# Kernel tuning notes

Measured on AMD Instinct MI355X. Metric: run time of the kernel, lower is better.

## Reference

```python
import jax, jax.numpy as jnp
import numpy as np

B, C, D, E = 2048, 64, 1024, 128
P_INT = 0.0  # p_int=0 -> intervention mask is all zeros (deterministic)


def setup_inputs() -> dict:
    key = jax.random.key(0)
    ks = jax.random.split(key, 16)
    s = lambda k, shape, fan: jax.random.normal(k, shape, jnp.float32) * (1.0 / np.sqrt(fan))
    return {
        "x": jax.random.normal(ks[0], (B, D), jnp.float32),
        "c_int": jax.random.uniform(ks[1], (B, C), jnp.float32),
        # stacked per-concept scorer MLP: Linear(D,D) -> ReLU -> Linear(D,1) -> Sigmoid
        "W1": s(ks[2], (C, D, D), D), "b1": jnp.zeros((C, D), jnp.float32),
        "w2": s(ks[3], (C, D), D), "b2": jnp.zeros((C,), jnp.float32),
        # stacked per-concept embed layer: Linear(D+1, D+1) -> ReLU
        "Wl": s(ks[4], (C, D + 1, D + 1), D + 1), "bl": jnp.zeros((C, D + 1), jnp.float32),
        # shared heads
        "Wmu": s(ks[5], (D + 1, E), D + 1), "bmu": jnp.zeros((E,), jnp.float32),
        "Wlv": s(ks[6], (D + 1, E), D + 1), "blv": jnp.zeros((E,), jnp.float32),
        "proto_pos": jax.random.normal(ks[7], (C, E), jnp.float32),
        "proto_neg": jax.random.normal(ks[8], (C, E), jnp.float32),
    }


def reference(x, c_int, W1, b1, w2, b2, Wl, bl, Wmu, bmu, Wlv, blv, proto_pos, proto_neg):
    # Concept scorers (all concepts batched as one grouped GEMM).
    h = jax.nn.relu(jnp.einsum("bd,cdk->bck", x, W1) + b1)          # [B,C,D]
    c_pred = jax.nn.sigmoid(jnp.einsum("bck,ck->bc", h, w2) + b2)    # [B,C]
    # Per-concept embedding layer on [x ; c_pred].
    xc = jnp.concatenate(
        [jnp.broadcast_to(x[:, None, :], (x.shape[0], C, D)), c_pred[..., None]], axis=-1
    )                                                                # [B,C,D+1]
    emb = jax.nn.relu(jnp.einsum("bck,ckj->bcj", xc, Wl) + bl)       # [B,C,D+1]
    mu = jnp.einsum("bcj,je->bce", emb, Wmu) + bmu                   # [B,C,E]
    logvar = jnp.einsum("bcj,je->bce", emb, Wlv) + blv               # [B,C,E]
    c_emb = mu  # eval mode: no reparameterization noise
    # Intervention blend (mask ~ Bernoulli(p_int); p_int=0 -> zeros, deterministic)
    mask = jnp.zeros_like(c_pred)                                    # [B,C]
    cp = mask * c_int + (1.0 - mask) * c_pred                        # [B,C]
    proto = cp[..., None] * proto_pos + (1.0 - cp[..., None]) * proto_neg  # [B,C,E]
    c_emb = mask[..., None] * proto + (1.0 - mask[..., None]) * c_emb
    return (c_pred, c_emb, mu, logvar)
```

## Files before the change

kernel.cpp:

```cpp
#include <hip/hip_runtime.h>
#include <hip/hip_bf16.h>
#include <cstdint>
#include <cstddef>

#define OFF_CE 131072ull
#define OFF_MU (131072ull + 16777216ull)
#define OFF_LV (131072ull + 33554432ull)

using bf16x8 = __attribute__((ext_vector_type(8))) __bf16;
using s16x8  = __attribute__((ext_vector_type(8))) short;
using f32x4  = __attribute__((ext_vector_type(4))) float;

__device__ __forceinline__ unsigned short f2bf(float x) {
  unsigned u = __builtin_bit_cast(unsigned, x);
  return (unsigned short)((u + 0x7FFFu + ((u >> 16) & 1u)) >> 16);
}
__device__ __forceinline__ float bf2f(unsigned short h) {
  unsigned u = ((unsigned)h) << 16;
  return __builtin_bit_cast(float, u);
}
__device__ __forceinline__ void async16(const void* g, void* l) {
  __builtin_amdgcn_global_load_lds(
      (const __attribute__((address_space(1))) void*)g,
      (__attribute__((address_space(3))) void*)l, 16, 0, 0);
}
__device__ __forceinline__ f32x4 nt_load4(const float* p4) {
  return __builtin_nontemporal_load((const f32x4*)p4);
}

struct PX {
  const float *Wl, *Wmu, *Wlv, *b2, *presum, *w2l, *bl1024, *Wlcolf;
  const unsigned short *xb;
  unsigned short *WlT, *WheadT;
  float *whead1024f, *e1024, *pred;
};

template <int ALIGNED, int NT>
__device__ __forceinline__ void tile_tr64(const float* __restrict__ src, int stride,
                                          unsigned short* __restrict__ dst, int t256,
                                          float (*t)[68]) {
#pragma unroll
  for (int i = 0; i < 4; ++i) {
    const int row = (t256 >> 4) + (i << 4);
    const int col4 = (t256 & 15) << 2;
    const float* sp = src + (size_t)row * stride + col4;
    f32x4 v;
    if constexpr (ALIGNED && NT) {
      v = nt_load4(sp);
    } else if constexpr (ALIGNED) {
      v = *(const f32x4*)sp;
    } else if constexpr (NT) {
      v.x = __builtin_nontemporal_load(sp);
      v.y = __builtin_nontemporal_load(sp + 1);
      v.z = __builtin_nontemporal_load(sp + 2);
      v.w = __builtin_nontemporal_load(sp + 3);
    } else {
      v.x = sp[0]; v.y = sp[1]; v.z = sp[2]; v.w = sp[3];
    }
    *(f32x4*)&t[row][col4] = v;
  }
  __syncthreads();
  const int n = t256 & 63;
#pragma unroll
  for (int pq = 0; pq < 2; ++pq) {
    const int k8 = ((t256 >> 6) << 3) + (pq << 5);
    unsigned short tmp[8];
#pragma unroll
    for (int j = 0; j < 8; ++j) tmp[j] = f2bf(t[k8 + j][n]);
    *(uint4*)(dst + (size_t)n * 1024 + k8) = *(uint4*)tmp;
  }
}

__global__ __launch_bounds__(256) void prep1_k(const float* __restrict__ W1,
                                               const float* __restrict__ x,
                                               const float* __restrict__ Wl,
                                               const float* __restrict__ bl,
                                               unsigned short* __restrict__ xb,
                                               unsigned short* __restrict__ W1T,
                                               float* __restrict__ wlastf,
                                               float* __restrict__ blpf,
                                               float* __restrict__ Wlcolf,
                                               float* __restrict__ w2l,
                                               float* __restrict__ bl1024) {
  __shared__ float t[64][68];
  const int bid = blockIdx.x;
  const int tid = threadIdx.x;
  if (bid < 16384) {
    const int c = bid >> 8, kt = (bid >> 4) & 15, nt = bid & 15;
    tile_tr64<1, 1>(W1 + ((size_t)c << 20) + ((size_t)(kt << 6) << 10) + (nt << 6), 1024,
                    W1T + ((size_t)c << 20) + ((size_t)(nt << 6) << 10) + (kt << 6), tid, t);
  } else if (bid < 17408) {
    const int idx = (bid - 16384) * 256 + tid;
    f32x4 a = nt_load4(x + (size_t)idx * 8);
    f32x4 b = nt_load4(x + (size_t)idx * 8 + 4);
    unsigned w0 = f2bf(a.x) | ((unsigned)f2bf(a.y) << 16);
    unsigned w1 = f2bf(a.z) | ((unsigned)f2bf(a.w) << 16);
    unsigned w2 = f2bf(b.x) | ((unsigned)f2bf(b.y) << 16);
    unsigned w3 = f2bf(b.z) | ((unsigned)f2bf(b.w) << 16);
    ((uint4*)xb)[idx] = make_uint4(w0, w1, w2, w3);
  } else {
    const int idx = (bid - 17408) * 256 + tid;
    const int c = idx >> 10, j = idx & 1023;
    const float* src = Wl + (size_t)c * 1050625;
    wlastf[idx] = __builtin_nontemporal_load(&src[(size_t)1024 * 1025 + j]);
    blpf[idx]   = bl[(size_t)c * 1025 + j];
    Wlcolf[idx] = __builtin_nontemporal_load(&src[(size_t)j * 1025 + 1024]);
    if (j == 0) {
      w2l[c]    = src[(size_t)1024 * 1025 + 1024];
      bl1024[c] = bl[(size_t)c * 1025 + 1024];
    }
  }
}

__device__ void tail_work(int e, int tid, char* lds, const PX& p) {
  if (e < 4096) {
    const int g = tid >> 8, t256 = tid & 255;
    const int tau0 = (e << 2) + (g << 1);
    float (*tA)[68] = (float(*)[68])(lds + g * 34816);
    float (*tB)[68] = (float(*)[68])(lds + g * 34816 + 17408);
    const int c0 = tau0 >> 8, kt0 = (tau0 >> 4) & 15, nt0 = tau0 & 15;
    const int tau1 = tau0 + 1;
    const int c1 = tau1 >> 8, kt1 = (tau1 >> 4) & 15, nt1 = tau1 & 15;
    const float* srcA = p.Wl + (size_t)c0 * 1050625 + (size_t)(kt0 << 6) * 1025 + (nt0 << 6);
    const float* srcB = p.Wl + (size_t)c1 * 1050625 + (size_t)(kt1 << 6) * 1025 + (nt1 << 6);
    unsigned short* dstA = p.WlT + ((size_t)c0 << 20) + ((size_t)(nt0 << 6) << 10) + (kt0 << 6);
    unsigned short* dstB = p.WlT + ((size_t)c1 << 20) + ((size_t)(nt1 << 6) << 10) + (kt1 << 6);
    const int row = t256 >> 4;
    const int col4 = (t256 & 15) << 2;
    f32x4 vA[4], vB[4];
#pragma unroll
    for (int i = 0; i < 4; ++i) {
      const float* q = srcA + (size_t)(row + (i << 4)) * 1025 + col4;
      vA[i].x = __builtin_nontemporal_load(q);
      vA[i].y = __builtin_nontemporal_load(q + 1);
      vA[i].z = __builtin_nontemporal_load(q + 2);
      vA[i].w = __builtin_nontemporal_load(q + 3);
    }
#pragma unroll
    for (int i = 0; i < 4; ++i) {
      const float* q = srcB + (size_t)(row + (i << 4)) * 1025 + col4;
      vB[i].x = __builtin_nontemporal_load(q);
      vB[i].y = __builtin_nontemporal_load(q + 1);
      vB[i].z = __builtin_nontemporal_load(q + 2);
      vB[i].w = __builtin_nontemporal_load(q + 3);
    }
#pragma unroll
    for (int i = 0; i < 4; ++i) *(f32x4*)&tA[row + (i << 4)][col4] = vA[i];
    __syncthreads();
#pragma unroll
    for (int i = 0; i < 4; ++i) *(f32x4*)&tB[row + (i << 4)][col4] = vB[i];
    const int n = t256 & 63;
#pragma unroll
    for (int pq = 0; pq < 2; ++pq) {
      const int k8 = ((t256 >> 6) << 3) + (pq << 5);
      unsigned short tmp[8];
#pragma unroll
      for (int j = 0; j < 8; ++j) tmp[j] = f2bf(tA[k8 + j][n]);
      *(uint4*)(dstA + (size_t)n * 1024 + k8) = *(uint4*)tmp;
    }
    __syncthreads();
#pragma unroll
    for (int pq = 0; pq < 2; ++pq) {
      const int k8 = ((t256 >> 6) << 3) + (pq << 5);
      unsigned short tmp[8];
#pragma unroll
      for (int j = 0; j < 8; ++j) tmp[j] = f2bf(tB[k8 + j][n]);
      *(uint4*)(dstB + (size_t)n * 1024 + k8) = *(uint4*)tmp;
    }
    return;
  }
  if (e < 4608) {
    const int we = e - 4096;
    const int idx = we * 512 + tid;
    const int rr = idx >> 10, k = idx & 1023;
    float v = (rr < 128) ? p.Wmu[(size_t)k * 128 + rr] : p.Wlv[(size_t)k * 128 + (rr - 128)];
    p.WheadT[idx] = f2bf(v);
    if (we == 0 && tid < 256)
      p.whead1024f[tid] = (tid < 128) ? p.Wmu[131072 + tid] : p.Wlv[131072 + (tid - 128)];
    return;
  }
  const int b = e - 4608;
  const int w = tid >> 6, lane = tid & 63;
  const unsigned short* xr = p.xb + ((size_t)b << 10) + lane * 16;
  s16x8 xv0 = *(const s16x8*)xr;
  s16x8 xv1 = *(const s16x8*)(xr + 8);
  float xf[16];
#pragma unroll
  for (int i = 0; i < 8; ++i) {
    xf[i] = bf2f((unsigned short)xv0[i]);
    xf[8 + i] = bf2f((unsigned short)xv1[i]);
  }
#pragma unroll
  for (int q = 0; q < 8; ++q) {
    const int c = (q << 3) + w;
    const float* wr = p.Wlcolf + (c << 10) + lane * 16;
    float s = 0.f;
#pragma unroll
    for (int q4 = 0; q4 < 4; ++q4) {
      f32x4 wv = *(const f32x4*)(wr + q4 * 4);
      s += xf[q4 * 4 + 0] * wv.x + xf[q4 * 4 + 1] * wv.y +
           xf[q4 * 4 + 2] * wv.z + xf[q4 * 4 + 3] * wv.w;
    }
#pragma unroll
    for (int off = 32; off; off >>= 1) s += __shfl_xor(s, off);
    if (lane == 0) ((float*)p.presum)[(c << 11) + b] = s;
  }
}


#define BAR() __builtin_amdgcn_s_barrier()
#define LGKM0() do { asm volatile("s_waitcnt lgkmcnt(0)" ::: "memory"); \
                     __builtin_amdgcn_sched_barrier(0); } while (0)
#define VM4() asm volatile("s_waitcnt vmcnt(4)" ::: "memory")
#define VM0() asm volatile("s_waitcnt vmcnt(0)" ::: "memory")

#define STAGEA(h, tt, bidx) do { _Pragma("unroll") for (int q_ = 0; q_ < 2; ++q_) \
  async16(Asrc[q_] + ((size_t)(h) * 128) * K + (size_t)(tt) * 64, \
          &sA[bidx][(h) * 8192 + chnk[q_]]); } while (0)
#define STAGEB(h, tt, bidx) do { _Pragma("unroll") for (int q_ = 0; q_ < 2; ++q_) \
  async16(Bsrc[q_] + ((size_t)(h) * 128) * K + (size_t)(tt) * 64, \
          &sB[bidx][(h) * 8192 + chnk[q_]]); } while (0)

#define LOADA(mh, bidx) do { _Pragma("unroll") for (int i_ = 0; i_ < 4; ++i_) { \
  const int ro_ = ((mh) * 128 + wm64 + i_ * 16 + l15) << 6; \
  a[i_][0] = *(const bf16x8*)&sA[bidx][ro_ + ccx0]; \
  a[i_][1] = *(const bf16x8*)&sA[bidx][ro_ + ccx1]; } } while (0)

#define LOADB(nh, bb, bidx) do { _Pragma("unroll") for (int j_ = 0; j_ < 2; ++j_) { \
  const int ro_ = ((nh) * 128 + wn32 + j_ * 16 + l15) << 6; \
  bb[j_][0] = *(const bf16x8*)&sB[bidx][ro_ + ccx0]; \
  bb[j_][1] = *(const bf16x8*)&sB[bidx][ro_ + ccx1]; } } while (0)

#define MMAQ(mh, nh, bb) do { _Pragma("unroll") for (int i_ = 0; i_ < 4; ++i_) \
  _Pragma("unroll") for (int j_ = 0; j_ < 2; ++j_) { \
    acc[(mh)*4+i_][(nh)*2+j_] = __builtin_amdgcn_mfma_f32_16x16x32_bf16( \
        a[i_][0], bb[j_][0], acc[(mh)*4+i_][(nh)*2+j_], 0, 0, 0); \
    acc[(mh)*4+i_][(nh)*2+j_] = __builtin_amdgcn_mfma_f32_16x16x32_bf16( \
        a[i_][1], bb[j_][1], acc[(mh)*4+i_][(nh)*2+j_], 0, 0, 0); \
  } } while (0)

#define KSTEP(t_, cb_, nb_) do { \
    LOADA(0, cb_); LOADB(0, b0, cb_); STAGEA(0, (t_) + 1, nb_); \
    BAR(); LGKM0(); \
    __builtin_amdgcn_s_setprio(1); MMAQ(0, 0, b0); __builtin_amdgcn_s_setprio(0); \
    VM4(); BAR(); \
    LOADB(1, b1, cb_); STAGEB(0, (t_) + 1, nb_); \
    BAR(); LGKM0(); \
    __builtin_amdgcn_s_setprio(1); MMAQ(0, 1, b1); __builtin_amdgcn_s_setprio(0); \
    VM4(); BAR(); \
    LOADA(1, cb_); STAGEB(1, (t_) + 1, nb_); \
    BAR(); LGKM0(); \
    __builtin_amdgcn_s_setprio(1); MMAQ(1, 1, b1); __builtin_amdgcn_s_setprio(0); \
    BAR(); \
    STAGEA(1, (t_) + 1, nb_); \
    BAR(); \
    __builtin_amdgcn_s_setprio(1); MMAQ(1, 0, b0); __builtin_amdgcn_s_setprio(0); \
    VM4(); BAR(); \
  } while (0)

template <int MODE, int K>
__global__ __launch_bounds__(512, 2) void gemm8p_k(
    const unsigned short* __restrict__ A, const unsigned short* __restrict__ BT,
    const float* __restrict__ e0, const float* __restrict__ e1,
    const float* __restrict__ e2, const float* __restrict__ e3,
    unsigned short* __restrict__ obf, float* __restrict__ ofl, PX p) {
  __shared__ unsigned short sA[2][16384];
  __shared__ unsigned short sB[2][16384];

  constexpr int GX = (MODE == 2) ? 1 : 4;
  constexpr int GY = (MODE == 2) ? 512 : 8;
  constexpr int NWG = GX * GY * ((MODE == 2) ? 1 : 64);

  const int tid = threadIdx.x;

  int rbid;
  if constexpr (MODE == 0) {
    const int bidR = blockIdx.x;
    if (bidR >= 2048) { tail_work(bidR - 2048, tid, (char*)&sA[0][0], p); return; }
    rbid = bidR;
  } else {
    rbid = blockIdx.x + GX * (blockIdx.y + GY * blockIdx.z);
  }

  const int lane = tid & 63;
  const int wid = tid >> 6;
  const int wm = wid >> 2, wn = wid & 3;
  const int l15 = lane & 15, l4 = lane >> 4;
  const int wm64 = wm << 6, wn32 = wn << 5;

  const int bid = (rbid & 7) * (NWG >> 3) + (rbid >> 3);
  const int bx = bid % GX;
  const int by = (bid / GX) % GY;
  const int c = bid / (GX * GY);

  const int n0 = bx << 8;
  const int m0 = by << 8;

  const unsigned short* Ab = A;
  const unsigned short* Bb;
  if constexpr (MODE == 2) Bb = BT;
  else                     Bb = BT + ((size_t)c << 20);

  int rloc[2], csrc[2], chnk[2];
  const unsigned short* Asrc[2];
  const unsigned short* Bsrc[2];
#pragma unroll
  for (int q = 0; q < 2; ++q) {
    const int s = ((wid << 1) + q) * 64 + lane;
    rloc[q] = s >> 3;
    csrc[q] = ((s & 7) ^ ((s >> 3) & 7)) << 3;
    chnk[q] = ((wid << 1) + q) << 9;
    Asrc[q] = Ab + (size_t)(m0 + rloc[q]) * K + csrc[q];
    Bsrc[q] = Bb + (size_t)(n0 + rloc[q]) * K + csrc[q];
  }

  const int xorv = l15 & 7;
  const int ccx0 = (l4 ^ xorv) << 3;
  const int ccx1 = ((4 + l4) ^ xorv) << 3;

  f32x4 acc[8][4];
#pragma unroll
  for (int i = 0; i < 8; ++i)
#pragma unroll
    for (int j = 0; j < 4; ++j) acc[i][j] = (f32x4)(0.f);

  bf16x8 a[4][2], b0[2][2], b1[2][2];

  static_assert(K == 1024, "schedule assumes 16 K-tiles");

  STAGEA(0, 0, 0); STAGEB(0, 0, 0); STAGEB(1, 0, 0); STAGEA(1, 0, 0);
  VM0();
  BAR();

#pragma unroll 1
  for (int tt = 0; tt < 7; ++tt) {
    const int t0 = tt << 1;
    KSTEP(t0, 0, 1);
    KSTEP(t0 + 1, 1, 0);
  }
  KSTEP(14, 0, 1);

  {
    VM0();
    BAR();
    LOADA(0, 1);
    LOADB(0, b0, 1);
    LGKM0();
    __builtin_amdgcn_s_setprio(1);
    MMAQ(0, 0, b0);
    __builtin_amdgcn_s_setprio(0);
    LOADB(1, b1, 1);
    LGKM0();
    __builtin_amdgcn_s_setprio(1);
    MMAQ(0, 1, b1);
    __builtin_amdgcn_s_setprio(0);
    LOADA(1, 1);
    LGKM0();
    __builtin_amdgcn_s_setprio(1);
    MMAQ(1, 1, b1);
    MMAQ(1, 0, b0);
    __builtin_amdgcn_s_setprio(0);
  }

  int coln[2][2];
#pragma unroll
  for (int nh = 0; nh < 2; ++nh)
#pragma unroll
    for (int j = 0; j < 2; ++j) coln[nh][j] = n0 + nh * 128 + wn32 + j * 16 + l15;

  if constexpr (MODE == 0) {
    float bias[2][2], w2v[2][2];
#pragma unroll
    for (int nh = 0; nh < 2; ++nh)
#pragma unroll
      for (int j = 0; j < 2; ++j) {
        bias[nh][j] = e0[(c << 10) + coln[nh][j]];
        w2v[nh][j]  = e1[(c << 10) + coln[nh][j]];
      }
    float* partL = (float*)&sA[0][0];
#pragma unroll
    for (int mh = 0; mh < 2; ++mh)
#pragma unroll
      for (int i = 0; i < 4; ++i)
#pragma unroll
        for (int rr = 0; rr < 4; ++rr) {
          float s = 0.f;
#pragma unroll
          for (int nh = 0; nh < 2; ++nh)
#pragma unroll
            for (int j = 0; j < 2; ++j) {
              float v = fmaxf(acc[mh * 4 + i][nh * 2 + j][rr] + bias[nh][j], 0.f);
              s += v * w2v[nh][j];
            }
          s += __shfl_xor(s, 1); s += __shfl_xor(s, 2);
          s += __shfl_xor(s, 4); s += __shfl_xor(s, 8);
          if (l15 == 0) partL[wid * 128 + mh * 64 + i * 16 + (l4 << 2) + rr] = s;
        }
    __syncthreads();
    if (tid < 256) {
      const int r = tid;
      const int mh_ = r >> 7, wmr = (r >> 6) & 1, low = r & 63;
      float s2 = 0.f;
#pragma unroll
      for (int wn2 = 0; wn2 < 4; ++wn2) s2 += partL[(wmr * 4 + wn2) * 128 + mh_ * 64 + low];
      ofl[(((size_t)(bx << 6) + c) << 11) + m0 + r] = s2;
    }
  } else if constexpr (MODE == 1) {
    float* cpL = (float*)&sA[0][0];
    if (tid < 256) {
      const int b = m0 + tid;
      float s = p.b2[c];
#pragma unroll
      for (int q = 0; q < 4; ++q) s += e2[(((size_t)(q << 6) + c) << 11) + b];
      float pv = 1.f / (1.f + expf(-s));
      cpL[tid] = pv;
      if (bx == 0) {
        p.pred[((size_t)b << 6) + c] = pv;
        p.e1024[(c << 11) + b] =
            fmaxf(p.presum[(c << 11) + b] + pv * p.w2l[c] + p.bl1024[c], 0.f);
      }
    }
    __syncthreads();
    float wl4[2][2], bb4[2][2];
#pragma unroll
    for (int nh = 0; nh < 2; ++nh)
#pragma unroll
      for (int j = 0; j < 2; ++j) {
        wl4[nh][j] = e0[(c << 10) + coln[nh][j]];
        bb4[nh][j] = e1[(c << 10) + coln[nh][j]];
      }
#pragma unroll
    for (int mh = 0; mh < 2; ++mh)
#pragma unroll
      for (int i = 0; i < 4; ++i)
#pragma unroll
        for (int rr = 0; rr < 4; ++rr) {
          const int rl = mh * 128 + wm64 + i * 16 + (l4 << 2) + rr;
          const int row = m0 + rl;
          const float cp = cpL[rl];
          unsigned short* orow = obf + (((size_t)(c << 11) + row) << 10);
#pragma unroll
          for (int nh = 0; nh < 2; ++nh)
#pragma unroll
            for (int j = 0; j < 2; ++j) {
              float v = acc[mh * 4 + i][nh * 2 + j][rr] + cp * wl4[nh][j] + bb4[nh][j];
              orow[coln[nh][j]] = f2bf(fmaxf(v, 0.f));
            }
        }
  } else {
    float bias[2][2], wh[2][2];
#pragma unroll
    for (int nh = 0; nh < 2; ++nh)
#pragma unroll
      for (int j = 0; j < 2; ++j) {
        bias[nh][j] = (nh == 0) ? e0[coln[0][j]] : e1[coln[1][j] - 128];
        wh[nh][j]   = e3[coln[nh][j]];
      }
#pragma unroll
    for (int mh = 0; mh < 2; ++mh)
#pragma unroll
      for (int i = 0; i < 4; ++i)
#pragma unroll
        for (int rr = 0; rr < 4; ++rr) {
          const int rid = m0 + mh * 128 + wm64 + i * 16 + (l4 << 2) + rr;
          const int cc = rid >> 11, b = rid & 2047;
          const float ev = e2[rid];
          const size_t ib = (((size_t)b << 6) + cc) << 7;
#pragma unroll
          for (int j = 0; j < 2; ++j) {
            float v = acc[mh * 4 + i][j][rr] + bias[0][j] + ev * wh[0][j];
            ofl[OFF_MU + ib + coln[0][j]] = v;
            ofl[OFF_CE + ib + coln[0][j]] = v;
          }
#pragma unroll
          for (int j = 0; j < 2; ++j) {
            float v = acc[mh * 4 + i][2 + j][rr] + bias[1][j] + ev * wh[1][j];
            ofl[OFF_LV + ib + (coln[1][j] - 128)] = v;
          }
        }
  }
}


extern "C" void kernel_launch(void* const* d_in, const int* in_sizes, int n_in,
                              void* d_out, int out_size, void* d_ws, size_t ws_size,
                              hipStream_t stream) {
  const float* x   = (const float*)d_in[0];
  const float* W1  = (const float*)d_in[2];
  const float* b1  = (const float*)d_in[3];
  const float* w2  = (const float*)d_in[4];
  const float* b2  = (const float*)d_in[5];
  const float* Wl  = (const float*)d_in[6];
  const float* bl  = (const float*)d_in[7];
  const float* Wmu = (const float*)d_in[8];
  const float* bmu = (const float*)d_in[9];
  const float* Wlv = (const float*)d_in[10];
  const float* blv = (const float*)d_in[11];
  float* out = (float*)d_out;

  char* ws = (char*)d_ws;
  size_t off = 0;
  auto take = [&](size_t bytes) { char* r = ws + off; off += bytes; return r; };
  unsigned short* xb     = (unsigned short*)take(4194304);
  unsigned short* W1T    = (unsigned short*)take(134217728);
  unsigned short* WlT    = (unsigned short*)take(134217728);
  float* wlastf          = (float*)take(262144);
  float* blpf            = (float*)take(262144);
  float* Wlcolf          = (float*)take(262144);
  float* w2l             = (float*)take(512);
  float* bl1024          = (float*)take(512);
  unsigned short* WheadT = (unsigned short*)take(524288);
  float* whead1024f      = (float*)take(1024);
  float* presum          = (float*)take(524288);
  float* spart           = (float*)take(2097152);
  float* e1024f          = (float*)take(524288);
  unsigned short* emb    = (unsigned short*)take(268435456);

  PX p;
  p.Wl = Wl; p.Wmu = Wmu; p.Wlv = Wlv; p.b2 = b2;
  p.presum = presum; p.w2l = w2l; p.bl1024 = bl1024; p.Wlcolf = Wlcolf;
  p.xb = xb; p.WlT = WlT; p.WheadT = WheadT;
  p.whead1024f = whead1024f; p.e1024 = e1024f; p.pred = out;

  prep1_k<<<17664, 256, 0, stream>>>(W1, x, Wl, bl, xb, W1T, wlastf, blpf, Wlcolf, w2l, bl1024);
  gemm8p_k<0, 1024><<<8704, 512, 0, stream>>>(xb, W1T, b1, w2, nullptr, nullptr,
                                              nullptr, spart, p);
  gemm8p_k<1, 1024><<<dim3(4, 8, 64), 512, 0, stream>>>(xb, WlT, wlastf, blpf, spart, nullptr,
                                                        emb, nullptr, p);
  gemm8p_k<2, 1024><<<dim3(1, 512, 1), 512, 0, stream>>>(emb, WheadT, bmu, blv, e1024f,
                                                         whead1024f, nullptr, out, p);
}
```

Before: 932.3 us.

## Split Wl transpose tail work out of GEMM into separate kernel; pair W1 tiles

Moves the Wl transpose, head-weight conversion and presum work out of the tail blocks of the first GEMM launch into a standalone kernel that runs between the two grouped GEMMs. Each block of the W1 prep kernel now has 512 threads and transposes two pairs of tiles, which cuts the block count. The goal is to keep low-occupancy transpose blocks from sharing the GEMM's 2-blocks-per-CU launch bounds and LDS footprint. The cost is an extra kernel launch and giving up any overlap of the memory-bound transpose with the compute-bound GEMM.

```diff
diff --git a/kernel.cpp b/kernel.cpp
--- a/kernel.cpp
+++ b/kernel.cpp
@@ -29,49 +29,68 @@
 }
 
 struct PX {
-  const float *Wl, *Wmu, *Wlv, *b2, *presum, *w2l, *bl1024, *Wlcolf;
-  const unsigned short *xb;
-  unsigned short *WlT, *WheadT;
-  float *whead1024f, *e1024, *pred;
+  const float *b2, *presum, *w2l, *bl1024;
+  float *e1024, *pred;
 };
 
-template <int ALIGNED, int NT>
-__device__ __forceinline__ void tile_tr64(const float* __restrict__ src, int stride,
-                                          unsigned short* __restrict__ dst, int t256,
-                                          float (*t)[68]) {
+template <int ALIGNED>
+__device__ __forceinline__ void tile_tr64_pair(
+    const float* __restrict__ srcA, const float* __restrict__ srcB, int stride,
+    unsigned short* __restrict__ dstA, unsigned short* __restrict__ dstB,
+    int t256, float (*tA)[68], float (*tB)[68]) {
+  const int row = t256 >> 4;
+  const int col4 = (t256 & 15) << 2;
+  f32x4 vA[4], vB[4];
 #pragma unroll
   for (int i = 0; i < 4; ++i) {
-    const int row = (t256 >> 4) + (i << 4);
-    const int col4 = (t256 & 15) << 2;
-    const float* sp = src + (size_t)row * stride + col4;
-    f32x4 v;
-    if constexpr (ALIGNED && NT) {
-      v = nt_load4(sp);
-    } else if constexpr (ALIGNED) {
-      v = *(const f32x4*)sp;
-    } else if constexpr (NT) {
-      v.x = __builtin_nontemporal_load(sp);
-      v.y = __builtin_nontemporal_load(sp + 1);
-      v.z = __builtin_nontemporal_load(sp + 2);
-      v.w = __builtin_nontemporal_load(sp + 3);
+    const float* q = srcA + (size_t)(row + (i << 4)) * stride + col4;
+    if constexpr (ALIGNED) {
+      vA[i] = nt_load4(q);
     } else {
-      v.x = sp[0]; v.y = sp[1]; v.z = sp[2]; v.w = sp[3];
-    }
-    *(f32x4*)&t[row][col4] = v;
-  }
+      vA[i].x = __builtin_nontemporal_load(q);
+      vA[i].y = __builtin_nontemporal_load(q + 1);
+      vA[i].z = __builtin_nontemporal_load(q + 2);
+      vA[i].w = __builtin_nontemporal_load(q + 3);
+    }
+  }
+#pragma unroll
+  for (int i = 0; i < 4; ++i) {
+    const float* q = srcB + (size_t)(row + (i << 4)) * stride + col4;
+    if constexpr (ALIGNED) {
+      vB[i] = nt_load4(q);
+    } else {
+      vB[i].x = __builtin_nontemporal_load(q);
+      vB[i].y = __builtin_nontemporal_load(q + 1);
+      vB[i].z = __builtin_nontemporal_load(q + 2);
+      vB[i].w = __builtin_nontemporal_load(q + 3);
+    }
+  }
+#pragma unroll
+  for (int i = 0; i < 4; ++i) *(f32x4*)&tA[row + (i << 4)][col4] = vA[i];
   __syncthreads();
+#pragma unroll
+  for (int i = 0; i < 4; ++i) *(f32x4*)&tB[row + (i << 4)][col4] = vB[i];
   const int n = t256 & 63;
 #pragma unroll
   for (int pq = 0; pq < 2; ++pq) {
     const int k8 = ((t256 >> 6) << 3) + (pq << 5);
     unsigned short tmp[8];
 #pragma unroll
-    for (int j = 0; j < 8; ++j) tmp[j] = f2bf(t[k8 + j][n]);
-    *(uint4*)(dst + (size_t)n * 1024 + k8) = *(uint4*)tmp;
-  }
-}
-
-__global__ __launch_bounds__(256) void prep1_k(const float* __restrict__ W1,
+    for (int j = 0; j < 8; ++j) tmp[j] = f2bf(tA[k8 + j][n]);
+    *(uint4*)(dstA + (size_t)n * 1024 + k8) = *(uint4*)tmp;
+  }
+  __syncthreads();
+#pragma unroll
+  for (int pq = 0; pq < 2; ++pq) {
+    const int k8 = ((t256 >> 6) << 3) + (pq << 5);
+    unsigned short tmp[8];
+#pragma unroll
+    for (int j = 0; j < 8; ++j) tmp[j] = f2bf(tB[k8 + j][n]);
+    *(uint4*)(dstB + (size_t)n * 1024 + k8) = *(uint4*)tmp;
+  }
+}
+
+__global__ __launch_bounds__(512) void prep1_k(const float* __restrict__ W1,
                                                const float* __restrict__ x,
                                                const float* __restrict__ Wl,
                                                const float* __restrict__ bl,
@@ -82,15 +101,23 @@
                                                float* __restrict__ Wlcolf,
                                                float* __restrict__ w2l,
                                                float* __restrict__ bl1024) {
-  __shared__ float t[64][68];
+  __shared__ float t[4][64][68];
   const int bid = blockIdx.x;
   const int tid = threadIdx.x;
-  if (bid < 16384) {
-    const int c = bid >> 8, kt = (bid >> 4) & 15, nt = bid & 15;
-    tile_tr64<1, 1>(W1 + ((size_t)c << 20) + ((size_t)(kt << 6) << 10) + (nt << 6), 1024,
-                    W1T + ((size_t)c << 20) + ((size_t)(nt << 6) << 10) + (kt << 6), tid, t);
-  } else if (bid < 17408) {
-    const int idx = (bid - 16384) * 256 + tid;
+  if (bid < 4096) {
+    const int g = tid >> 8, t256 = tid & 255;
+    const int tau0 = (bid << 2) + (g << 1);
+    const int c0 = tau0 >> 8, kt0 = (tau0 >> 4) & 15, nt0 = tau0 & 15;
+    const int tau1 = tau0 + 1;
+    const int c1 = tau1 >> 8, kt1 = (tau1 >> 4) & 15, nt1 = tau1 & 15;
+    tile_tr64_pair<1>(
+        W1 + ((size_t)c0 << 20) + ((size_t)(kt0 << 6) << 10) + (nt0 << 6),
+        W1 + ((size_t)c1 << 20) + ((size_t)(kt1 << 6) << 10) + (nt1 << 6), 1024,
+        W1T + ((size_t)c0 << 20) + ((size_t)(nt0 << 6) << 10) + (kt0 << 6),
+        W1T + ((size_t)c1 << 20) + ((size_t)(nt1 << 6) << 10) + (kt1 << 6),
+        t256, t[g << 1], t[(g << 1) + 1]);
+  } else if (bid < 4608) {
+    const int idx = (bid - 4096) * 512 + tid;
     f32x4 a = nt_load4(x + (size_t)idx * 8);
     f32x4 b = nt_load4(x + (size_t)idx * 8 + 4);
     unsigned w0 = f2bf(a.x) | ((unsigned)f2bf(a.y) << 16);
@@ -99,7 +126,7 @@
     unsigned w3 = f2bf(b.z) | ((unsigned)f2bf(b.w) << 16);
     ((uint4*)xb)[idx] = make_uint4(w0, w1, w2, w3);
   } else {
-    const int idx = (bid - 17408) * 256 + tid;
+    const int idx = (bid - 4608) * 512 + tid;
     const int c = idx >> 10, j = idx & 1023;
     const float* src = Wl + (size_t)c * 1050625;
     wlastf[idx] = __builtin_nontemporal_load(&src[(size_t)1024 * 1025 + j]);
@@ -112,98 +139,65 @@
   }
 }
 
-__device__ void tail_work(int e, int tid, char* lds, const PX& p) {
-  if (e < 4096) {
+__global__ __launch_bounds__(512) void wl2_k(const float* __restrict__ Wl,
+                                             const float* __restrict__ Wmu,
+                                             const float* __restrict__ Wlv,
+                                             const unsigned short* __restrict__ xb,
+                                             const float* __restrict__ Wlcolf,
+                                             unsigned short* __restrict__ WlT,
+                                             unsigned short* __restrict__ WheadT,
+                                             float* __restrict__ whead1024f,
+                                             float* __restrict__ presum) {
+  __shared__ float t[4][64][68];
+  const int bid = blockIdx.x;
+  const int tid = threadIdx.x;
+  if (bid < 4096) {
     const int g = tid >> 8, t256 = tid & 255;
-    const int tau0 = (e << 2) + (g << 1);
-    float (*tA)[68] = (float(*)[68])(lds + g * 34816);
-    float (*tB)[68] = (float(*)[68])(lds + g * 34816 + 17408);
+    const int tau0 = (bid << 2) + (g << 1);
     const int c0 = tau0 >> 8, kt0 = (tau0 >> 4) & 15, nt0 = tau0 & 15;
     const int tau1 = tau0 + 1;
     const int c1 = tau1 >> 8, kt1 = (tau1 >> 4) & 15, nt1 = tau1 & 15;
-    const float* srcA = p.Wl + (size_t)c0 * 1050625 + (size_t)(kt0 << 6) * 1025 + (nt0 << 6);
-    const float* srcB = p.Wl + (size_t)c1 * 1050625 + (size_t)(kt1 << 6) * 1025 + (nt1 << 6);
-    unsigned short* dstA = p.WlT + ((size_t)c0 << 20) + ((size_t)(nt0 << 6) << 10) + (kt0 << 6);
-    unsigned short* dstB = p.WlT + ((size_t)c1 << 20) + ((size_t)(nt1 << 6) << 10) + (kt1 << 6);
-    const int row = t256 >> 4;
-    const int col4 = (t256 & 15) << 2;
-    f32x4 vA[4], vB[4];
-#pragma unroll
-    for (int i = 0; i < 4; ++i) {
-      const float* q = srcA + (size_t)(row + (i << 4)) * 1025 + col4;
-      vA[i].x = __builtin_nontemporal_load(q);
-      vA[i].y = __builtin_nontemporal_load(q + 1);
-      vA[i].z = __builtin_nontemporal_load(q + 2);
-      vA[i].w = __builtin_nontemporal_load(q + 3);
-    }
-#pragma unroll
-    for (int i = 0; i < 4; ++i) {
-      const float* q = srcB + (size_t)(row + (i << 4)) * 1025 + col4;
-      vB[i].x = __builtin_nontemporal_load(q);
-      vB[i].y = __builtin_nontemporal_load(q + 1);
-      vB[i].z = __builtin_nontemporal_load(q + 2);
-      vB[i].w = __builtin_nontemporal_load(q + 3);
-    }
-#pragma unroll
-    for (int i = 0; i < 4; ++i) *(f32x4*)&tA[row + (i << 4)][col4] = vA[i];
-    __syncthreads();
-#pragma unroll
-    for (int i = 0; i < 4; ++i) *(f32x4*)&tB[row + (i << 4)][col4] = vB[i];
-    const int n = t256 & 63;
-#pragma unroll
-    for (int pq = 0; pq < 2; ++pq) {
-      const int k8 = ((t256 >> 6) << 3) + (pq << 5);
-      unsigned short tmp[8];
-#pragma unroll
-      for (int j = 0; j < 8; ++j) tmp[j] = f2bf(tA[k8 + j][n]);
-      *(uint4*)(dstA + (size_t)n * 1024 + k8) = *(uint4*)tmp;
-    }
-    __syncthreads();
-#pragma unroll
-    for (int pq = 0; pq < 2; ++pq) {
-      const int k8 = ((t256 >> 6) << 3) + (pq << 5);
-      unsigned short tmp[8];
-#pragma unroll
-      for (int j = 0; j < 8; ++j) tmp[j] = f2bf(tB[k8 + j][n]);
-      *(uint4*)(dstB + (size_t)n * 1024 + k8) = *(uint4*)tmp;
-    }
-    return;
-  }
-  if (e < 4608) {
-    const int we = e - 4096;
+    tile_tr64_pair<0>(
+        Wl + (size_t)c0 * 1050625 + (size_t)(kt0 << 6) * 1025 + (nt0 << 6),
+        Wl + (size_t)c1 * 1050625 + (size_t)(kt1 << 6) * 1025 + (nt1 << 6), 1025,
+        WlT + ((size_t)c0 << 20) + ((size_t)(nt0 << 6) << 10) + (kt0 << 6),
+        WlT + ((size_t)c1 << 20) + ((size_t)(nt1 << 6) << 10) + (kt1 << 6),
+        t256, t[g << 1], t[(g << 1) + 1]);
+  } else if (bid < 4608) {
+    const int we = bid - 4096;
     const int idx = we * 512 + tid;
     const int rr = idx >> 10, k = idx & 1023;
-    float v = (rr < 128) ? p.Wmu[(size_t)k * 128 + rr] : p.Wlv[(size_t)k * 128 + (rr - 128)];
-    p.WheadT[idx] = f2bf(v);
+    float v = (rr < 128) ? Wmu[(size_t)k * 128 + rr] : Wlv[(size_t)k * 128 + (rr - 128)];
+    WheadT[idx] = f2bf(v);
     if (we == 0 && tid < 256)
-      p.whead1024f[tid] = (tid < 128) ? p.Wmu[131072 + tid] : p.Wlv[131072 + (tid - 128)];
-    return;
-  }
-  const int b = e - 4608;
-  const int w = tid >> 6, lane = tid & 63;
-  const unsigned short* xr = p.xb + ((size_t)b << 10) + lane * 16;
-  s16x8 xv0 = *(const s16x8*)xr;
-  s16x8 xv1 = *(const s16x8*)(xr + 8);
-  float xf[16];
-#pragma unroll
-  for (int i = 0; i < 8; ++i) {
-    xf[i] = bf2f((unsigned short)xv0[i]);
-    xf[8 + i] = bf2f((unsigned short)xv1[i]);
-  }
-#pragma unroll
-  for (int q = 0; q < 8; ++q) {
-    const int c = (q << 3) + w;
-    const float* wr = p.Wlcolf + (c << 10) + lane * 16;
-    float s = 0.f;
-#pragma unroll
-    for (int q4 = 0; q4 < 4; ++q4) {
-      f32x4 wv = *(const f32x4*)(wr + q4 * 4);
-      s += xf[q4 * 4 + 0] * wv.x + xf[q4 * 4 + 1] * wv.y +
-           xf[q4 * 4 + 2] * wv.z + xf[q4 * 4 + 3] * wv.w;
-    }
-#pragma unroll
-    for (int off = 32; off; off >>= 1) s += __shfl_xor(s, off);
-    if (lane == 0) ((float*)p.presum)[(c << 11) + b] = s;
+      whead1024f[tid] = (tid < 128) ? Wmu[131072 + tid] : Wlv[131072 + (tid - 128)];
+  } else {
+    const int b = bid - 4608;
+    const int w = tid >> 6, lane = tid & 63;
+    const unsigned short* xr = xb + ((size_t)b << 10) + lane * 16;
+    s16x8 xv0 = *(const s16x8*)xr;
+    s16x8 xv1 = *(const s16x8*)(xr + 8);
+    float xf[16];
+#pragma unroll
+    for (int i = 0; i < 8; ++i) {
+      xf[i] = bf2f((unsigned short)xv0[i]);
+      xf[8 + i] = bf2f((unsigned short)xv1[i]);
+    }
+#pragma unroll
+    for (int q = 0; q < 8; ++q) {
+      const int c = (q << 3) + w;
+      const float* wr = Wlcolf + (c << 10) + lane * 16;
+      float s = 0.f;
+#pragma unroll
+      for (int q4 = 0; q4 < 4; ++q4) {
+        f32x4 wv = *(const f32x4*)(wr + q4 * 4);
+        s += xf[q4 * 4 + 0] * wv.x + xf[q4 * 4 + 1] * wv.y +
+             xf[q4 * 4 + 2] * wv.z + xf[q4 * 4 + 3] * wv.w;
+      }
+#pragma unroll
+      for (int off = 32; off; off >>= 1) s += __shfl_xor(s, off);
+      if (lane == 0) presum[(c << 11) + b] = s;
+    }
   }
 }
 
@@ -272,22 +266,13 @@
   constexpr int NWG = GX * GY * ((MODE == 2) ? 1 : 64);
 
   const int tid = threadIdx.x;
-
-  int rbid;
-  if constexpr (MODE == 0) {
-    const int bidR = blockIdx.x;
-    if (bidR >= 2048) { tail_work(bidR - 2048, tid, (char*)&sA[0][0], p); return; }
-    rbid = bidR;
-  } else {
-    rbid = blockIdx.x + GX * (blockIdx.y + GY * blockIdx.z);
-  }
-
   const int lane = tid & 63;
   const int wid = tid >> 6;
   const int wm = wid >> 2, wn = wid & 3;
   const int l15 = lane & 15, l4 = lane >> 4;
   const int wm64 = wm << 6, wn32 = wn << 5;
 
+  const int rbid = blockIdx.x + GX * (blockIdx.y + GY * blockIdx.z);
   const int bid = (rbid & 7) * (NWG >> 3) + (rbid >> 3);
   const int bx = bid % GX;
   const int by = (bid / GX) % GY;
@@ -517,14 +502,13 @@
   unsigned short* emb    = (unsigned short*)take(268435456);
 
   PX p;
-  p.Wl = Wl; p.Wmu = Wmu; p.Wlv = Wlv; p.b2 = b2;
-  p.presum = presum; p.w2l = w2l; p.bl1024 = bl1024; p.Wlcolf = Wlcolf;
-  p.xb = xb; p.WlT = WlT; p.WheadT = WheadT;
-  p.whead1024f = whead1024f; p.e1024 = e1024f; p.pred = out;
-
-  prep1_k<<<17664, 256, 0, stream>>>(W1, x, Wl, bl, xb, W1T, wlastf, blpf, Wlcolf, w2l, bl1024);
-  gemm8p_k<0, 1024><<<8704, 512, 0, stream>>>(xb, W1T, b1, w2, nullptr, nullptr,
-                                              nullptr, spart, p);
+  p.b2 = b2; p.presum = presum; p.w2l = w2l; p.bl1024 = bl1024;
+  p.e1024 = e1024f; p.pred = out;
+
+  prep1_k<<<4736, 512, 0, stream>>>(W1, x, Wl, bl, xb, W1T, wlastf, blpf, Wlcolf, w2l, bl1024);
+  gemm8p_k<0, 1024><<<dim3(4, 8, 64), 512, 0, stream>>>(xb, W1T, b1, w2, nullptr, nullptr,
+                                                        nullptr, spart, p);
+  wl2_k<<<6656, 512, 0, stream>>>(Wl, Wmu, Wlv, xb, Wlcolf, WlT, WheadT, whead1024f, presum);
   gemm8p_k<1, 1024><<<dim3(4, 8, 64), 512, 0, stream>>>(xb, WlT, wlastf, blpf, spart, nullptr,
                                                         emb, nullptr, p);
   gemm8p_k<2, 1024><<<dim3(1, 512, 1), 512, 0, stream>>>(emb, WheadT, bmu, blv, e1024f,
```

Result: no change. 948.8 us (+1.8%).
